# Optimization experiments

Measured on AMD Instinct MI355X. Metric: run time of the kernel, lower is better.

The kernel has to match this reference:

```python
import jax, jax.numpy as jnp
import numpy as np

EMBED = 2048
HEADS = 16
HEAD_DIM = EMBED // HEADS


def setup_inputs() -> dict:
    key = jax.random.key(0)
    ks = jax.random.split(key, 9)
    s = 1.0 / np.sqrt(EMBED)
    inp = {"x": jax.random.normal(ks[0], (2, 2048, EMBED), dtype=jnp.float32)}
    for i, name in enumerate(["q", "k", "v", "o"]):
        inp[f"W{name}"] = jax.random.uniform(ks[1 + 2 * i], (EMBED, EMBED), dtype=jnp.float32, minval=-s, maxval=s)
        inp[f"b{name}"] = jax.random.uniform(ks[2 + 2 * i], (EMBED,), dtype=jnp.float32, minval=-s, maxval=s)
    return inp


def reference(x, Wq, bq, Wk, bk, Wv, bv, Wo, bo):
    B, S, E = x.shape
    def split_heads(t):
        return t.reshape(B, S, HEADS, HEAD_DIM).transpose(0, 2, 1, 3)  # [B,H,S,D]
    q = split_heads(x @ Wq.T + bq)
    k = split_heads(x @ Wk.T + bk)
    v = split_heads(x @ Wv.T + bv)
    scale = 1.0 / np.sqrt(HEAD_DIM)
    scores = jnp.einsum("bhqd,bhkd->bhqk", q, k) * scale  # [B,H,S,S]
    causal = jnp.tril(jnp.ones((S, S), dtype=bool))
    scores = jnp.where(causal[None, None], scores, -jnp.inf)
    attn = jax.nn.softmax(scores, axis=-1)
    out = jnp.einsum("bhqk,bhkd->bhqd", attn, v)  # [B,H,S,D]
    out = out.transpose(0, 2, 1, 3).reshape(B, S, E)
    return out @ Wo.T + bo
```

## Files before the change

kernel.cpp:

```cpp
#include <hip/hip_runtime.h>

typedef unsigned short u16;
typedef unsigned int u32;
typedef __attribute__((ext_vector_type(8))) short bf16x8;
typedef __attribute__((ext_vector_type(4))) float f32x4;

#define MFMA(a, b, c) __builtin_amdgcn_mfma_f32_16x16x32_bf16((a), (b), (c), 0, 0, 0)

__device__ inline u16 f2bf(float f) {
  u32 u = __float_as_uint(f);
  u = (u + 0x7fffu + ((u >> 16) & 1u)) >> 16;
  return (u16)u;
}

__device__ inline void gld16(u16* lds, const u16* g) {
  __builtin_amdgcn_global_load_lds((const __attribute__((address_space(1))) void*)g,
                                   (__attribute__((address_space(3))) void*)lds,
                                   16, 0, 0);
}

__global__ __launch_bounds__(256) void cvt_all(const float* __restrict__ x,
                                               const float* __restrict__ wa,
                                               const float* __restrict__ wb,
                                               const float* __restrict__ wc,
                                               const float* __restrict__ wd,
                                               uint2* __restrict__ dst) {
  int i = blockIdx.x * 256 + threadIdx.x;
  const float* s;
  int off;
  if (i < 2097152) {
    s = x; off = i;
  } else {
    int j = i - 2097152;
    int which = j >> 20;
    off = j & 1048575;
    s = (which == 0) ? wa : (which == 1) ? wb : (which == 2) ? wc : wd;
  }
  float4 f = ((const float4*)s)[off];
  u32 lo = (u32)f2bf(f.x) | ((u32)f2bf(f.y) << 16);
  u32 hi = (u32)f2bf(f.z) | ((u32)f2bf(f.w) << 16);
  dst[i] = make_uint2(lo, hi);
}

__device__ inline void gemm_core(const u16* __restrict__ A, const u16* __restrict__ W,
                                 u16* As, u16* Bs, int m0, int n0, f32x4 acc[4][4]) {
  const int K = 2048;
  const int NT = 64;
  int t = threadIdx.x, w = t >> 6, l = t & 63;
  int wr = (w >> 1) * 64, wc = (w & 1) * 64;
  int fr = l & 15, fg = l >> 4;
  int r0 = t >> 2;
  int r1 = 64 + r0;
  int c00 = (t & 3) ^ ((r0 >> 1) & 3);
  int c01 = (t & 3) ^ ((r1 >> 1) & 3);
  const u16* gA = A + (size_t)m0 * K;
  const u16* gB = W + (size_t)n0 * K;
  size_t a0 = (size_t)r0 * K + c00 * 8;
  size_t a1 = (size_t)r1 * K + c01 * 8;
#pragma unroll
  for (int p = 0; p < 2; ++p) {
    u16* sa = As + p * 4096;
    u16* sb = Bs + p * 4096;
    int kk = p * 32;
    gld16(sa + w * 512, gA + a0 + kk);
    gld16(sa + 2048 + w * 512, gA + a1 + kk);
    gld16(sb + w * 512, gB + a0 + kk);
    gld16(sb + 2048 + w * 512, gB + a1 + kk);
  }
  for (int kt = 0; kt < NT; ++kt) {
    int kt2 = (kt + 2 < NT) ? (kt + 2) : (NT - 1);
    u16* sa = As + ((kt + 2) & 3) * 4096;
    u16* sb = Bs + ((kt + 2) & 3) * 4096;
    int kk = kt2 * 32;
    gld16(sa + w * 512, gA + a0 + kk);
    gld16(sa + 2048 + w * 512, gA + a1 + kk);
    gld16(sb + w * 512, gB + a0 + kk);
    gld16(sb + 2048 + w * 512, gB + a1 + kk);
    asm volatile("s_waitcnt vmcnt(8)\n\ts_barrier" ::: "memory");
    const u16* ca = As + (kt & 3) * 4096;
    const u16* cb = Bs + (kt & 3) * 4096;
    bf16x8 af[4], bfv[4];
#pragma unroll
    for (int i = 0; i < 4; ++i) {
      int ar = wr + i * 16 + fr;
      af[i] = *(const bf16x8*)&ca[ar * 32 + ((fg ^ ((ar >> 1) & 3)) << 3)];
    }
#pragma unroll
    for (int i = 0; i < 4; ++i) {
      int br = wc + i * 16 + fr;
      bfv[i] = *(const bf16x8*)&cb[br * 32 + ((fg ^ ((br >> 1) & 3)) << 3)];
    }
#pragma unroll
    for (int mi = 0; mi < 4; ++mi)
#pragma unroll
      for (int ni = 0; ni < 4; ++ni)
        acc[mi][ni] = MFMA(af[mi], bfv[ni], acc[mi][ni]);
  }
}

__global__ __launch_bounds__(256, 2) void qkv_gemm(
    const u16* __restrict__ X, const u16* __restrict__ Wq, const u16* __restrict__ Wk,
    const u16* __restrict__ Wv, const float* __restrict__ bq, const float* __restrict__ bk,
    const float* __restrict__ bv, u16* __restrict__ Qo, u16* __restrict__ Ko,
    u16* __restrict__ Vo) {
  __shared__ __attribute__((aligned(16))) u16 As[16384];
  __shared__ __attribute__((aligned(16))) u16 Bs[16384];
  int which = blockIdx.x >> 4;
  int n0 = (blockIdx.x & 15) * 128;
  int m0 = blockIdx.y * 128;
  const u16* W = (which == 0) ? Wq : (which == 1) ? Wk : Wv;
  const float* bias = (which == 0) ? bq : (which == 1) ? bk : bv;
  u16* out = (which == 0) ? Qo : (which == 1) ? Ko : Vo;
  float scale = (which == 0) ? 0.08838834764831845f : 1.0f;
  f32x4 zero4 = {0.f, 0.f, 0.f, 0.f};
  f32x4 acc[4][4];
#pragma unroll
  for (int i = 0; i < 4; ++i)
#pragma unroll
    for (int j = 0; j < 4; ++j) acc[i][j] = zero4;
  gemm_core(X, W, As, Bs, m0, n0, acc);
  int t = threadIdx.x, w = t >> 6, l = t & 63;
  int wr = (w >> 1) * 64, wc = (w & 1) * 64;
  if (which == 2) {
#pragma unroll
    for (int mi = 0; mi < 4; ++mi) {
#pragma unroll
      for (int ni = 0; ni < 4; ++ni) {
        int row = m0 + wr + mi * 16 + (l >> 4) * 4;
        int col = n0 + wc + ni * 16 + (l & 15);
        float bb = bias[col];
        int h = col >> 7, d = col & 127;
        int b = row >> 11, s = row & 2047;
        u32 p0 = (u32)f2bf(acc[mi][ni][0] + bb) | ((u32)f2bf(acc[mi][ni][1] + bb) << 16);
        u32 p1 = (u32)f2bf(acc[mi][ni][2] + bb) | ((u32)f2bf(acc[mi][ni][3] + bb) << 16);
        *(uint2*)&out[((size_t)(b * 16 + h) * 128 + d) * 2048 + s] = make_uint2(p0, p1);
      }
    }
  } else {
#pragma unroll
    for (int mi = 0; mi < 4; ++mi) {
#pragma unroll
      for (int ni = 0; ni < 4; ++ni) {
        int row = m0 + wr + mi * 16 + (l >> 4) * 4;
        int col = n0 + wc + ni * 16 + (l & 15);
        float bb = bias[col];
        int h = col >> 7, d = col & 127;
#pragma unroll
        for (int i = 0; i < 4; ++i) {
          int m = row + i;
          int b = m >> 11, s = m & 2047;
          float v = (acc[mi][ni][i] + bb) * scale;
          out[(((size_t)b * 16 + h) * 2048 + s) * 128 + d] = f2bf(v);
        }
      }
    }
  }
}

__global__ __launch_bounds__(256, 2) void oproj_gemm(const u16* __restrict__ A,
                                                     const u16* __restrict__ W,
                                                     const float* __restrict__ bias,
                                                     float* __restrict__ out) {
  __shared__ __attribute__((aligned(16))) u16 As[16384];
  __shared__ __attribute__((aligned(16))) u16 Bs[16384];
  int n0 = blockIdx.x * 128, m0 = blockIdx.y * 128;
  f32x4 zero4 = {0.f, 0.f, 0.f, 0.f};
  f32x4 acc[4][4];
#pragma unroll
  for (int i = 0; i < 4; ++i)
#pragma unroll
    for (int j = 0; j < 4; ++j) acc[i][j] = zero4;
  gemm_core(A, W, As, Bs, m0, n0, acc);
  int t = threadIdx.x, w = t >> 6, l = t & 63;
  int wr = (w >> 1) * 64, wc = (w & 1) * 64;
#pragma unroll
  for (int mi = 0; mi < 4; ++mi) {
#pragma unroll
    for (int ni = 0; ni < 4; ++ni) {
      int row = m0 + wr + mi * 16 + (l >> 4) * 4;
      int col = n0 + wc + ni * 16 + (l & 15);
      float bb = bias[col];
#pragma unroll
      for (int i = 0; i < 4; ++i) out[(size_t)(row + i) * 2048 + col] = acc[mi][ni][i] + bb;
    }
  }
}

__global__ __launch_bounds__(256, 2) void attn_fwd(const u16* __restrict__ Q,
                                                   const u16* __restrict__ K,
                                                   const u16* __restrict__ Vt,
                                                   u16* __restrict__ AO) {
  __shared__ __attribute__((aligned(16))) u16 Ks[8192];
  __shared__ __attribute__((aligned(16))) u16 Vts[8192];
  __shared__ __attribute__((aligned(16))) u16 Pl[8192];
  const int D = 128;
  int b3 = blockIdx.x;
  int bh = b3 & 31;
  int xq = b3 >> 5;
  int qt = (xq < 8) ? (15 - xq) : (xq - 8);
  int t = threadIdx.x, w = t >> 6, l = t & 63, g = l >> 4, c = l & 15;
  size_t base = (size_t)bh * 2048 * 128;
  const u16* Vbh = Vt + base;
  int q0 = qt * 128;
  int qrw = q0 + w * 32;
  bf16x8 qf[2][4];
#pragma unroll
  for (int mi = 0; mi < 2; ++mi) {
    const u16* qp = Q + base + (size_t)(qrw + mi * 16 + c) * D + g * 8;
#pragma unroll
    for (int ks = 0; ks < 4; ++ks) qf[mi][ks] = *(const bf16x8*)(qp + ks * 32);
  }
  f32x4 zero4 = {0.f, 0.f, 0.f, 0.f};
  f32x4 oacc[2][8];
#pragma unroll
  for (int mi = 0; mi < 2; ++mi)
#pragma unroll
    for (int i = 0; i < 8; ++i) oacc[mi][i] = zero4;
  float mrow[2][4], lrow[2][4];
#pragma unroll
  for (int mi = 0; mi < 2; ++mi)
#pragma unroll
    for (int i = 0; i < 4; ++i) { mrow[mi][i] = -1e30f; lrow[mi][i] = 0.f; }
  char* pw = (char*)(Pl + w * 2048);
  int ktmax = 2 * qt + 1;
  for (int kt = 0; kt <= ktmax; ++kt) {
    int kv0 = kt * 64;
    __syncthreads();
#pragma unroll
    for (int ci = 0; ci < 4; ++ci) {
      int row = w * 16 + ci * 4 + g;
      int cc = c ^ (row & 7);
      gld16(Ks + w * 2048 + ci * 512, K + base + (size_t)(kv0 + row) * D + cc * 8);
    }
#pragma unroll
    for (int ci = 0; ci < 4; ++ci) {
      int vr = ci * 32 + w * 8 + (l >> 3);
      int vslot = (l & 7) ^ ((l >> 3) & 7);
      gld16(Vts + ci * 2048 + w * 512, Vbh + (size_t)vr * 2048 + kv0 + vslot * 8);
    }
    __syncthreads();
    if (kv0 <= qrw + 31) {
      f32x4 sacc[2][4];
#pragma unroll
      for (int mi = 0; mi < 2; ++mi)
#pragma unroll
        for (int n = 0; n < 4; ++n) sacc[mi][n] = zero4;
#pragma unroll
      for (int ks = 0; ks < 4; ++ks) {
#pragma unroll
        for (int n = 0; n < 4; ++n) {
          int row = n * 16 + c;
          bf16x8 kf = *(const bf16x8*)&Ks[row * 128 + (((ks * 4 + g) ^ (c & 7)) << 3)];
          sacc[0][n] = MFMA(qf[0][ks], kf, sacc[0][n]);
          sacc[1][n] = MFMA(qf[1][ks], kf, sacc[1][n]);
        }
      }
      float sc[2][4][4];
#pragma unroll
      for (int mi = 0; mi < 2; ++mi)
#pragma unroll
        for (int n = 0; n < 4; ++n)
#pragma unroll
          for (int i = 0; i < 4; ++i) sc[mi][n][i] = sacc[mi][n][i];
      if (kv0 + 63 > qrw) {
#pragma unroll
        for (int mi = 0; mi < 2; ++mi)
#pragma unroll
          for (int n = 0; n < 4; ++n) {
            int kv = kv0 + n * 16 + c;
#pragma unroll
            for (int i = 0; i < 4; ++i)
              if (kv > qrw + mi * 16 + g * 4 + i) sc[mi][n][i] = -1e30f;
          }
      }
      float tmax[2][4];
#pragma unroll
      for (int mi = 0; mi < 2; ++mi)
#pragma unroll
        for (int i = 0; i < 4; ++i)
          tmax[mi][i] = fmaxf(fmaxf(sc[mi][0][i], sc[mi][1][i]), fmaxf(sc[mi][2][i], sc[mi][3][i]));
#pragma unroll
      for (int x = 1; x < 16; x <<= 1)
#pragma unroll
        for (int mi = 0; mi < 2; ++mi)
#pragma unroll
          for (int i = 0; i < 4; ++i) tmax[mi][i] = fmaxf(tmax[mi][i], __shfl_xor(tmax[mi][i], x));
      float corr[2][4], rs[2][4];
#pragma unroll
      for (int mi = 0; mi < 2; ++mi)
#pragma unroll
        for (int i = 0; i < 4; ++i) {
          float mn = fmaxf(mrow[mi][i], tmax[mi][i]);
          corr[mi][i] = __expf(mrow[mi][i] - mn);
          mrow[mi][i] = mn;
          rs[mi][i] = 0.f;
        }
      float ps[2][4][4];
#pragma unroll
      for (int mi = 0; mi < 2; ++mi)
#pragma unroll
        for (int n = 0; n < 4; ++n)
#pragma unroll
          for (int i = 0; i < 4; ++i) {
            ps[mi][n][i] = __expf(sc[mi][n][i] - mrow[mi][i]);
            rs[mi][i] += ps[mi][n][i];
          }
#pragma unroll
      for (int x = 1; x < 16; x <<= 1)
#pragma unroll
        for (int mi = 0; mi < 2; ++mi)
#pragma unroll
          for (int i = 0; i < 4; ++i) rs[mi][i] += __shfl_xor(rs[mi][i], x);
#pragma unroll
      for (int mi = 0; mi < 2; ++mi)
#pragma unroll
        for (int i = 0; i < 4; ++i) lrow[mi][i] = lrow[mi][i] * corr[mi][i] + rs[mi][i];
#pragma unroll
      for (int mi = 0; mi < 2; ++mi)
#pragma unroll
        for (int nf = 0; nf < 8; ++nf)
#pragma unroll
          for (int i = 0; i < 4; ++i) oacc[mi][nf][i] *= corr[mi][i];
#pragma unroll
      for (int mi = 0; mi < 2; ++mi)
#pragma unroll
        for (int n = 0; n < 4; ++n)
#pragma unroll
          for (int i = 0; i < 4; ++i) {
            int row = mi * 16 + g * 4 + i;
            *(u16*)(pw + row * 128 + ((n * 32 + c * 2) ^ ((row & 7) << 4))) = f2bf(ps[mi][n][i]);
          }
#pragma unroll
      for (int ks = 0; ks < 2; ++ks) {
        bf16x8 pf0 = *(const bf16x8*)(pw + (c)*128 + ((ks * 64 + g * 16) ^ ((c & 7) << 4)));
        bf16x8 pf1 = *(const bf16x8*)(pw + (16 + c) * 128 + ((ks * 64 + g * 16) ^ ((c & 7) << 4)));
#pragma unroll
        for (int nf = 0; nf < 8; ++nf) {
          bf16x8 vf = *(const bf16x8*)&Vts[(nf * 16 + c) * 64 + (((ks * 4 + g) ^ (c & 7)) << 3)];
          oacc[0][nf] = MFMA(pf0, vf, oacc[0][nf]);
          oacc[1][nf] = MFMA(pf1, vf, oacc[1][nf]);
        }
      }
    }
  }
  int b = bh >> 4, h = bh & 15;
#pragma unroll
  for (int mi = 0; mi < 2; ++mi)
#pragma unroll
    for (int nf = 0; nf < 8; ++nf) {
      int d = h * 128 + nf * 16 + c;
#pragma unroll
      for (int i = 0; i < 4; ++i) {
        int q = qrw + mi * 16 + g * 4 + i;
        AO[((size_t)b * 2048 + q) * 2048 + d] = f2bf(oacc[mi][nf][i] / lrow[mi][i]);
      }
    }
}

extern "C" void kernel_launch(void* const* d_in, const int* in_sizes, int n_in,
                              void* d_out, int out_size, void* d_ws, size_t ws_size,
                              hipStream_t stream) {
  const float* x = (const float*)d_in[0];
  const float* Wq = (const float*)d_in[1];
  const float* bq = (const float*)d_in[2];
  const float* Wk = (const float*)d_in[3];
  const float* bk = (const float*)d_in[4];
  const float* Wv = (const float*)d_in[5];
  const float* bv = (const float*)d_in[6];
  const float* Wo = (const float*)d_in[7];
  const float* bo = (const float*)d_in[8];
  float* out = (float*)d_out;

  u16* xb = (u16*)d_ws;
  u16* Wqb = xb + 8388608;
  u16* Wkb = Wqb + 4194304;
  u16* Wvb = Wkb + 4194304;
  u16* Wob = Wvb + 4194304;
  u16* Qb = Wob + 4194304;
  u16* Kb = Qb + 8388608;
  u16* Vb = Kb + 8388608;
  u16* AOb = xb;

  cvt_all<<<24576, 256, 0, stream>>>(x, Wq, Wk, Wv, Wo, (uint2*)d_ws);
  qkv_gemm<<<dim3(48, 32), 256, 0, stream>>>(xb, Wqb, Wkb, Wvb, bq, bk, bv, Qb, Kb, Vb);
  attn_fwd<<<512, 256, 0, stream>>>(Qb, Kb, Vb, AOb);
  oproj_gemm<<<dim3(16, 32), 256, 0, stream>>>(AOb, Wob, bo, out);
}
```

Baseline: 289.5 us.

## Enlarge QKV GEMM tiles to 256x256 with 512-thread blocks and MFMA priority

The QKV projection GEMM now uses 256x256 output tiles computed by 8 waves, each covering 128x64, in place of 128x128 tiles with 4 waves. The K-loop is inlined with a 4-stage LDS ring buffer. s_setprio is raised around the MFMA block, in both the shared gemm_core and the new loop. The larger tiles are meant to raise operand reuse and cut global traffic per FLOP. In exchange, the kernel needs 128KB of LDS per block, uses more accumulator registers, and launches only 384 blocks, so occupancy may drop.

Result: no change. 286.6 us (-1.0%).

```diff
diff --git a/kernel.cpp b/kernel.cpp
--- a/kernel.cpp
+++ b/kernel.cpp
@@ -90,44 +90,94 @@
       int br = wc + i * 16 + fr;
       bfv[i] = *(const bf16x8*)&cb[br * 32 + ((fg ^ ((br >> 1) & 3)) << 3)];
     }
+    __builtin_amdgcn_s_setprio(1);
 #pragma unroll
     for (int mi = 0; mi < 4; ++mi)
 #pragma unroll
       for (int ni = 0; ni < 4; ++ni)
         acc[mi][ni] = MFMA(af[mi], bfv[ni], acc[mi][ni]);
-  }
-}
-
-__global__ __launch_bounds__(256, 2) void qkv_gemm(
+    __builtin_amdgcn_s_setprio(0);
+  }
+}
+
+__global__ __launch_bounds__(512, 2) void qkv_gemm(
     const u16* __restrict__ X, const u16* __restrict__ Wq, const u16* __restrict__ Wk,
     const u16* __restrict__ Wv, const float* __restrict__ bq, const float* __restrict__ bk,
     const float* __restrict__ bv, u16* __restrict__ Qo, u16* __restrict__ Ko,
     u16* __restrict__ Vo) {
-  __shared__ __attribute__((aligned(16))) u16 As[16384];
-  __shared__ __attribute__((aligned(16))) u16 Bs[16384];
-  int which = blockIdx.x >> 4;
-  int n0 = (blockIdx.x & 15) * 128;
-  int m0 = blockIdx.y * 128;
+  __shared__ __attribute__((aligned(16))) u16 As[32768];
+  __shared__ __attribute__((aligned(16))) u16 Bs[32768];
+  const int K = 2048, NT = 64;
+  int which = blockIdx.x >> 3;
+  int n0 = (blockIdx.x & 7) * 256;
+  int m0 = blockIdx.y * 256;
   const u16* W = (which == 0) ? Wq : (which == 1) ? Wk : Wv;
   const float* bias = (which == 0) ? bq : (which == 1) ? bk : bv;
   u16* out = (which == 0) ? Qo : (which == 1) ? Ko : Vo;
   float scale = (which == 0) ? 0.08838834764831845f : 1.0f;
+  int t = threadIdx.x, w = t >> 6, l = t & 63;
+  int wm = w >> 2, wn = w & 3;
+  int fr = l & 15, fg = l >> 4;
+  int r0 = t >> 2;
+  int c0 = (t & 3) ^ ((r0 >> 1) & 3);
+  const u16* gA = X + (size_t)m0 * K;
+  const u16* gB = W + (size_t)n0 * K;
+  size_t a0 = (size_t)r0 * K + c0 * 8;
+  size_t a1 = a0 + (size_t)128 * K;
   f32x4 zero4 = {0.f, 0.f, 0.f, 0.f};
-  f32x4 acc[4][4];
-#pragma unroll
-  for (int i = 0; i < 4; ++i)
+  f32x4 acc[8][4];
+#pragma unroll
+  for (int i = 0; i < 8; ++i)
 #pragma unroll
     for (int j = 0; j < 4; ++j) acc[i][j] = zero4;
-  gemm_core(X, W, As, Bs, m0, n0, acc);
-  int t = threadIdx.x, w = t >> 6, l = t & 63;
-  int wr = (w >> 1) * 64, wc = (w & 1) * 64;
+#pragma unroll
+  for (int p = 0; p < 2; ++p) {
+    u16* sa = As + p * 8192;
+    u16* sb = Bs + p * 8192;
+    int kk = p * 32;
+    gld16(sa + w * 512, gA + a0 + kk);
+    gld16(sa + 4096 + w * 512, gA + a1 + kk);
+    gld16(sb + w * 512, gB + a0 + kk);
+    gld16(sb + 4096 + w * 512, gB + a1 + kk);
+  }
+  for (int kt = 0; kt < NT; ++kt) {
+    int kt2 = (kt + 2 < NT) ? (kt + 2) : (NT - 1);
+    u16* sa = As + ((kt + 2) & 3) * 8192;
+    u16* sb = Bs + ((kt + 2) & 3) * 8192;
+    int kk = kt2 * 32;
+    gld16(sa + w * 512, gA + a0 + kk);
+    gld16(sa + 4096 + w * 512, gA + a1 + kk);
+    gld16(sb + w * 512, gB + a0 + kk);
+    gld16(sb + 4096 + w * 512, gB + a1 + kk);
+    asm volatile("s_waitcnt vmcnt(8)\n\ts_barrier" ::: "memory");
+    const u16* ca = As + (kt & 3) * 8192;
+    const u16* cb = Bs + (kt & 3) * 8192;
+    bf16x8 af[8], bfv[4];
+#pragma unroll
+    for (int i = 0; i < 8; ++i) {
+      int ar = wm * 128 + i * 16 + fr;
+      af[i] = *(const bf16x8*)&ca[ar * 32 + ((fg ^ ((ar >> 1) & 3)) << 3)];
+    }
+#pragma unroll
+    for (int i = 0; i < 4; ++i) {
+      int br = wn * 64 + i * 16 + fr;
+      bfv[i] = *(const bf16x8*)&cb[br * 32 + ((fg ^ ((br >> 1) & 3)) << 3)];
+    }
+    __builtin_amdgcn_s_setprio(1);
+#pragma unroll
+    for (int mi = 0; mi < 8; ++mi)
+#pragma unroll
+      for (int ni = 0; ni < 4; ++ni)
+        acc[mi][ni] = MFMA(af[mi], bfv[ni], acc[mi][ni]);
+    __builtin_amdgcn_s_setprio(0);
+  }
   if (which == 2) {
 #pragma unroll
-    for (int mi = 0; mi < 4; ++mi) {
+    for (int mi = 0; mi < 8; ++mi) {
 #pragma unroll
       for (int ni = 0; ni < 4; ++ni) {
-        int row = m0 + wr + mi * 16 + (l >> 4) * 4;
-        int col = n0 + wc + ni * 16 + (l & 15);
+        int row = m0 + wm * 128 + mi * 16 + (l >> 4) * 4;
+        int col = n0 + wn * 64 + ni * 16 + (l & 15);
         float bb = bias[col];
         int h = col >> 7, d = col & 127;
         int b = row >> 11, s = row & 2047;
@@ -138,11 +188,11 @@
     }
   } else {
 #pragma unroll
-    for (int mi = 0; mi < 4; ++mi) {
+    for (int mi = 0; mi < 8; ++mi) {
 #pragma unroll
       for (int ni = 0; ni < 4; ++ni) {
-        int row = m0 + wr + mi * 16 + (l >> 4) * 4;
-        int col = n0 + wc + ni * 16 + (l & 15);
+        int row = m0 + wm * 128 + mi * 16 + (l >> 4) * 4;
+        int col = n0 + wn * 64 + ni * 16 + (l & 15);
         float bb = bias[col];
         int h = col >> 7, d = col & 127;
 #pragma unroll
@@ -382,7 +432,7 @@
   u16* AOb = xb;
 
   cvt_all<<<24576, 256, 0, stream>>>(x, Wq, Wk, Wv, Wo, (uint2*)d_ws);
-  qkv_gemm<<<dim3(48, 32), 256, 0, stream>>>(xb, Wqb, Wkb, Wvb, bq, bk, bv, Qb, Kb, Vb);
+  qkv_gemm<<<dim3(24, 16), 512, 0, stream>>>(xb, Wqb, Wkb, Wvb, bq, bk, bv, Qb, Kb, Vb);
   attn_fwd<<<512, 256, 0, stream>>>(Qb, Kb, Vb, AOb);
   oproj_gemm<<<dim3(16, 32), 256, 0, stream>>>(AOb, Wob, bo, out);
 }
```
